# Performance work log

Measured on AMD Instinct MI355X. Metric: run time of the kernel, lower is better.

The kernel has to match this reference:

```python
import jax, jax.numpy as jnp
import numpy as np
from functools import partial

PI = 3.141592653589793

def prelu(x, a):
    return jnp.where(x > 0, x, a.reshape(()) * x)

def conv(x, w, b, stride=1):
    # torch Conv2d(k=3, padding=1): explicit (1,1) padding
    y = jax.lax.conv_general_dilated(
        x, w, window_strides=(stride, stride), padding=((1, 1), (1, 1)),
        dimension_numbers=("NCHW", "OIHW", "NCHW"))
    return y + b[None, :, None, None]

def feature_extractor(x, p):
    x = prelu(conv(x, p["w1"], p["b1"], 1), p["a1"])
    x1 = prelu(conv(x, p["w2"], p["b2"], 1), p["a2"])
    x = prelu(conv(x1, p["w3"], p["b3"], 2), p["a3"])
    x2 = prelu(conv(x, p["w4"], p["b4"], 1), p["a4"])
    x = prelu(conv(x2, p["w5"], p["b5"], 2), p["a5"])
    x3 = prelu(conv(x, p["w6"], p["b6"], 1), p["a6"])
    return x1, x2, x3

def cal_inter_flow(flo, sigma, t):
    # quadratic flow interpolation: circular-arc model with chord d, half-angle beta
    fx, fy = flo[:, 0:1], flo[:, 1:2]
    alpha = jnp.arctan2(fy, fx)
    beta = jnp.arcsin(sigma)
    d = jnp.sqrt(fx * fx + fy * fy)
    mask = jnp.abs(sigma) < 0.01            # near-linear motion branch
    safe_sig = jnp.where(mask, 1.0, sigma)
    R = jnp.where(mask, 0.0, d / (2.0 * safe_sig))
    th0 = alpha + PI / 2 + beta
    th1 = alpha + PI / 2 - beta
    tht = th0 + (th1 - th0) * t
    ftx = jnp.where(mask, t * fx, R * (jnp.cos(tht) - jnp.cos(th0)))
    fty = jnp.where(mask, t * fy, R * (jnp.sin(tht) - jnp.sin(th0)))
    return jnp.concatenate([ftx, fty], axis=1)

def flow_scale(flo, shape):
    # F.interpolate(bilinear, align_corners=False) then rescale flow magnitudes
    B = flo.shape[0]
    h, w = shape
    f = jax.image.resize(flo, (B, 2, h, w), method="bilinear")
    scale = jnp.asarray([w / flo.shape[3], h / flo.shape[2]], f.dtype).reshape(1, 2, 1, 1)
    return f * scale

def forward_warp(feat, flow):
    # 'average' forward splatting: bilinear scatter-add of values and weights, then normalize
    B, C, H, W = feat.shape
    gy, gx = jnp.meshgrid(jnp.arange(H, dtype=feat.dtype), jnp.arange(W, dtype=feat.dtype), indexing="ij")
    tx = gx[None] + flow[:, 0]              # [B,H,W] target coords
    ty = gy[None] + flow[:, 1]
    x0 = jnp.floor(tx); y0 = jnp.floor(ty)
    dx = tx - x0; dy = ty - y0
    x0i = x0.astype(jnp.int32); y0i = y0.astype(jnp.int32)
    featf = feat.reshape(B, C, H * W)
    num = jnp.zeros((B, C, H * W), feat.dtype)
    den = jnp.zeros((B, 1, H * W), feat.dtype)
    bidx = jnp.arange(B)[:, None, None]
    cidx = jnp.arange(C)[None, :, None]
    c0 = jnp.zeros((1, 1, 1), jnp.int32)
    corners = [
        (x0i,     y0i,     (1 - dx) * (1 - dy)),
        (x0i + 1, y0i,     dx * (1 - dy)),
        (x0i,     y0i + 1, (1 - dx) * dy),
        (x0i + 1, y0i + 1, dx * dy),
    ]
    for xi, yi, wgt in corners:
        valid = (xi >= 0) & (xi < W) & (yi >= 0) & (yi < H)
        wgt = (wgt * valid).reshape(B, 1, H * W)
        idx = (jnp.clip(yi, 0, H - 1) * W + jnp.clip(xi, 0, W - 1)).reshape(B, 1, H * W)
        num = num.at[bidx, cidx, idx].add(featf * wgt)
        den = den.at[bidx, c0, idx].add(wgt)
    out = num / jnp.maximum(den, 1e-7)
    return out.reshape(B, C, H, W)

def _forward(img0, img1, flow01, sigma01, flow10, sigma10, p):
    t = 0.5
    mean = jnp.concatenate([img0, img1], 1).mean(axis=(1, 2, 3), keepdims=True)
    img0 = img0 - mean
    img1 = img1 - mean
    flow_0t = cal_inter_flow(flow01, sigma01, t)
    flow_1t = cal_inter_flow(flow10, sigma10, 1 - t)
    f01, f02, f03 = feature_extractor(img0, p)
    f11, f12, f13 = feature_extractor(img1, p)
    fl0_d = flow_scale(flow_0t, f01.shape[2:]); fl1_d = flow_scale(flow_1t, f11.shape[2:])
    fl0_dd = flow_scale(flow_0t, f02.shape[2:]); fl1_dd = flow_scale(flow_1t, f12.shape[2:])
    fl0_ddd = flow_scale(flow_0t, f03.shape[2:]); fl1_ddd = flow_scale(flow_1t, f13.shape[2:])
    img_0t = forward_warp(img0, fl0_d);  img_1t = forward_warp(img1, fl1_d)
    ft0_1 = forward_warp(f01, fl0_d);    ft1_1 = forward_warp(f11, fl1_d)
    ft0_2 = forward_warp(f02, fl0_dd);   ft1_2 = forward_warp(f12, fl1_dd)
    ft0_3 = forward_warp(f03, fl0_ddd);  ft1_3 = forward_warp(f13, fl1_ddd)
    sig_0t = forward_warp(sigma01, flow_0t); sig_1t = forward_warp(sigma10, flow_1t)
    outs = [
        jnp.concatenate([img_0t, img_1t], 1),
        jnp.concatenate([ft0_1, ft1_1], 1),
        jnp.concatenate([ft0_2, ft1_2], 1),
        jnp.concatenate([ft0_3, ft1_3], 1),
        jnp.concatenate([sig_0t, sig_1t], 1),
    ]
    return jnp.concatenate([o.reshape(-1) for o in outs])

def setup_inputs() -> dict:
    key = jax.random.key(0)
    ks = jax.random.split(key, 16)
    B, H, W = 4, 256, 448
    inp = {
        "img0": jax.random.normal(ks[0], (B, 3, H, W), jnp.float32),
        "img1": jax.random.normal(ks[1], (B, 3, H, W), jnp.float32),
        "flow01": jax.random.normal(ks[2], (B, 2, H, W), jnp.float32) * 3.0,
        "sigma01": jax.random.uniform(ks[3], (B, 1, H, W), jnp.float32, -0.9, 0.9),
        "flow10": jax.random.normal(ks[4], (B, 2, H, W), jnp.float32) * 3.0,
        "sigma10": jax.random.uniform(ks[5], (B, 1, H, W), jnp.float32, -0.9, 0.9),
    }
    chans = [(32, 3), (32, 32), (64, 32), (64, 64), (96, 64), (96, 96)]
    for i, (o, c) in enumerate(chans, 1):
        inp[f"w{i}"] = jax.random.normal(ks[5 + i], (o, c, 3, 3), jnp.float32) * 0.05
        inp[f"b{i}"] = jnp.zeros((o,), jnp.float32)
        inp[f"a{i}"] = 0.25 * jnp.ones((1,), jnp.float32)
    return inp

def reference(img0, img1, flow01, sigma01, flow10, sigma10,
              w1, b1, a1, w2, b2, a2, w3, b3, a3,
              w4, b4, a4, w5, b5, a5, w6, b6, a6):
    p = dict(w1=w1, b1=b1, a1=a1, w2=w2, b2=b2, a2=a2, w3=w3, b3=b3, a3=a3,
             w4=w4, b4=b4, a4=a4, w5=w5, b5=b5, a5=a5, w6=w6, b6=b6, a6=a6)
    return _forward(img0, img1, flow01, sigma01, flow10, sigma10, p)
```

## Files before the change

### kernel.cpp

```cpp
#include <hip/hip_runtime.h>
#include <hip/hip_fp16.h>

static constexpr int B  = 4;
static constexpr int H0 = 256, W0 = 448, HW0 = H0 * W0;
static constexpr int H1 = 128, W1 = 224, HW1 = H1 * W1;
static constexpr int H2 = 64,  W2 = 112, HW2 = H2 * W2;

typedef _Float16 half8_t __attribute__((ext_vector_type(8)));
typedef _Float16 half4_t __attribute__((ext_vector_type(4)));
typedef float floatx4 __attribute__((ext_vector_type(4)));

static constexpr int NC_F = (W0 + 1) * (H0 + 1);
static constexpr int NC_H = (W1 + 1) * (H1 + 1);
static constexpr int NC_Q = (W2 + 1) * (H2 + 1);

static constexpr int RS_F = 20;
static constexpr int RS_H = 36;
static constexpr int RS_Q = 52;

static constexpr int SZ_F = 2 * B * NC_F;
static constexpr int SZ_H = 2 * B * NC_H;
static constexpr int SZ_Q = 2 * B * NC_Q;
static constexpr int CNT_TOTAL = SZ_F + SZ_H + SZ_Q;

static constexpr int CHUNK = 16384;
static constexpr int NCH_F = (SZ_F + CHUNK - 1) / CHUNK;
static constexpr int NCH_H = (SZ_H + CHUNK - 1) / CHUNK;
static constexpr int NCH_Q = (SZ_Q + CHUNK - 1) / CHUNK;
static constexpr int NCHUNKS = NCH_F + NCH_H + NCH_Q;

static constexpr size_t OFF_MEAN   = 0;
static constexpr size_t OFF_CNT    = 256;
static constexpr size_t ZERO_FLOATS = OFF_CNT + CNT_TOTAL;
static constexpr size_t OFF_BUFA   = ZERO_FLOATS;
static constexpr size_t OFF_BUFB   = OFF_BUFA + (size_t)4 * 32 * HW0;
static constexpr size_t OFF_FLOW   = OFF_BUFB + (size_t)4 * 32 * HW0;
static constexpr size_t OFF_FLH    = OFF_FLOW + (size_t)2 * B * 2 * HW0;
static constexpr size_t OFF_FLQ    = OFF_FLH + (size_t)2 * B * 2 * HW1;
static constexpr size_t OFF_WT2 = OFF_FLQ + (size_t)2 * B * 2 * HW2;
static constexpr size_t OFF_WT3 = OFF_WT2 + 4608;
static constexpr size_t OFF_WT4 = OFF_WT3 + 9216;
static constexpr size_t OFF_WT5 = OFF_WT4 + 18432;
static constexpr size_t OFF_WT6 = OFF_WT5 + 27648;
static constexpr size_t OFF_CS   = OFF_WT6 + 41472;
static constexpr size_t OFF_CURS = OFF_CS + (size_t)2 * CNT_TOTAL;
static constexpr size_t OFF_TPRE = OFF_CURS + CNT_TOTAL;
static constexpr size_t OFF_PSUM = OFF_TPRE + (size_t)NCHUNKS * 256;
static constexpr size_t OFF_RECS = OFF_PSUM + 128;
static constexpr size_t WS_FLOATS = OFF_RECS + (size_t)2 * B * HW0 * RS_F;

static constexpr size_t O_IMG = 0;
static constexpr size_t O_F1  = O_IMG + (size_t)B * 6 * HW0;
static constexpr size_t O_F2  = O_F1  + (size_t)B * 64 * HW0;
static constexpr size_t O_F3  = O_F2  + (size_t)B * 128 * HW1;
static constexpr size_t O_SIG = O_F3  + (size_t)B * 192 * HW2;

__device__ inline void h2f(unsigned u, float& lo, float& hi) {
  __half2 h = *reinterpret_cast<__half2*>(&u);
  float2 f = __half22float2(h);
  lo = f.x; hi = f.y;
}
__device__ inline unsigned f2h(float lo, float hi) {
  __half2 h = __floats2half2_rn(lo, hi);
  return *reinterpret_cast<unsigned*>(&h);
}

__device__ inline void chunk_map(int b, int& off, int& sz, int& ci) {
  if (b < NCH_F)              { off = 0;           sz = SZ_F; ci = b; }
  else if (b < NCH_F + NCH_H) { off = SZ_F;        sz = SZ_H; ci = b - NCH_F; }
  else                        { off = SZ_F + SZ_H; sz = SZ_Q; ci = b - NCH_F - NCH_H; }
}

__global__ __launch_bounds__(256) void k_mean(const float* __restrict__ img0,
                                              const float* __restrict__ img1,
                                              float* __restrict__ msum, int perImg) {
  int b = blockIdx.y;
  float s = 0.f;
  int tot = 2 * perImg;
  for (int i = blockIdx.x * blockDim.x + threadIdx.x; i < tot; i += gridDim.x * blockDim.x) {
    s += (i < perImg) ? img0[(size_t)b * perImg + i] : img1[(size_t)b * perImg + (i - perImg)];
  }
#pragma unroll
  for (int o = 32; o > 0; o >>= 1) s += __shfl_down(s, o);
  __shared__ float red[4];
  int lane = threadIdx.x & 63, wid = threadIdx.x >> 6;
  if (lane == 0) red[wid] = s;
  __syncthreads();
  if (threadIdx.x == 0) atomicAdd(&msum[b], red[0] + red[1] + red[2] + red[3]);
}

__global__ __launch_bounds__(256) void k_interflow2(
    const float* __restrict__ f01, const float* __restrict__ s01,
    const float* __restrict__ f10, const float* __restrict__ s10,
    float* __restrict__ outBase, unsigned* __restrict__ cntF) {
  constexpr int NCX = W0 + 1;
  int i = blockIdx.x * 256 + threadIdx.x;
  if (i >= 2 * B * HW0) return;
  int nb = i / HW0;
  int px = i - nb * HW0;
  int dir = nb >> 2, b = nb & 3;
  const float* flo = dir ? f10 : f01;
  const float* sigma = dir ? s10 : s01;
  float fx = flo[((size_t)(b * 2 + 0)) * HW0 + px];
  float fy = flo[((size_t)(b * 2 + 1)) * HW0 + px];
  float sg = sigma[(size_t)b * HW0 + px];
  float ftx, fty;
  if (fabsf(sg) < 0.01f) {
    ftx = 0.5f * fx; fty = 0.5f * fy;
  } else {
    float g = (1.f - sqrtf(fmaxf(0.f, 1.f - sg * sg))) / (2.f * sg);
    ftx = 0.5f * fx - g * fy;
    fty = 0.5f * fy + g * fx;
  }
  outBase[((size_t)(nb * 2 + 0)) * HW0 + px] = ftx;
  outBase[((size_t)(nb * 2 + 1)) * HW0 + px] = fty;
  int sw = px % W0, sh = px / W0;
  float tx = (float)sw + ftx, ty = (float)sh + fty;
  int x0 = (int)floorf(tx), y0 = (int)floorf(ty);
  if (x0 >= -1 && x0 <= W0 - 1 && y0 >= -1 && y0 <= H0 - 1)
    atomicAdd(&cntF[nb * NC_F + (y0 + 1) * NCX + (x0 + 1)], 1u);
}

template <int F, int Hd, int Wd>
__global__ __launch_bounds__(256) void k_downflow2(
    const float* __restrict__ in, float* __restrict__ out,
    unsigned* __restrict__ cnt) {
  constexpr int HWd = Hd * Wd;
  constexpr int NCX = Wd + 1;
  constexpr int NC  = (Wd + 1) * (Hd + 1);
  int i = blockIdx.x * 256 + threadIdx.x;
  if (i >= 2 * B * HWd) return;
  int nb = i / HWd;
  int px = i - nb * HWd;
  int ow = px % Wd, oh = px / Wd;
  float cy = (oh + 0.5f) * F - 0.5f;
  float cx = (ow + 0.5f) * F - 0.5f;
  int ylo = (int)floorf(cy) - F + 1;
  int xlo = (int)floorf(cx) - F + 1;
  const float* ipx = in + ((size_t)(nb * 2 + 0)) * HW0;
  const float* ipy = in + ((size_t)(nb * 2 + 1)) * HW0;
  float ax = 0.f, ay = 0.f, wn = 0.f;
  for (int jy = 0; jy < 2 * F; jy++) {
    int y = ylo + jy;
    if ((unsigned)y >= (unsigned)H0) continue;
    float wy = 1.f - fabsf((float)y - cy) / (float)F;
    for (int jx = 0; jx < 2 * F; jx++) {
      int x = xlo + jx;
      if ((unsigned)x >= (unsigned)W0) continue;
      float wx = 1.f - fabsf((float)x - cx) / (float)F;
      float ww = wy * wx;
      ax += ww * ipx[(size_t)y * W0 + x];
      ay += ww * ipy[(size_t)y * W0 + x];
      wn += ww;
    }
  }
  float s = 1.f / (wn * (float)F);
  float fx = ax * s, fy = ay * s;
  out[((size_t)(nb * 2 + 0)) * HWd + px] = fx;
  out[((size_t)(nb * 2 + 1)) * HWd + px] = fy;
  float tx = (float)ow + fx, ty = (float)oh + fy;
  int x0 = (int)floorf(tx), y0 = (int)floorf(ty);
  if (x0 >= -1 && x0 <= Wd - 1 && y0 >= -1 && y0 <= Hd - 1)
    atomicAdd(&cnt[nb * NC + (y0 + 1) * NCX + (x0 + 1)], 1u);
}

__global__ __launch_bounds__(256) void k_wtrans_all(
    const float* __restrict__ w2, const float* __restrict__ w3,
    const float* __restrict__ w4, const float* __restrict__ w5,
    const float* __restrict__ w6,
    _Float16* __restrict__ o2, _Float16* __restrict__ o3,
    _Float16* __restrict__ o4, _Float16* __restrict__ o5,
    _Float16* __restrict__ o6) {
  int i = blockIdx.x * 256 + threadIdx.x;
  const float* w; _Float16* o; int COUT, CIN, base;
  if      (i <   9216) { w = w2; o = o2; COUT = 32; CIN = 32; base = 0; }
  else if (i <  27648) { w = w3; o = o3; COUT = 64; CIN = 32; base = 9216; }
  else if (i <  64512) { w = w4; o = o4; COUT = 64; CIN = 64; base = 27648; }
  else if (i < 119808) { w = w5; o = o5; COUT = 96; CIN = 64; base = 64512; }
  else if (i < 202752) { w = w6; o = o6; COUT = 96; CIN = 96; base = 119808; }
  else return;
  int j = i - base;
  int q = j % 9;
  int rest = j / 9;
  int ci = rest % CIN;
  int co = rest / CIN;
  o[((size_t)q * COUT + co) * CIN + ci] = (_Float16)w[j];
}

__global__ __launch_bounds__(256) void conv1_nhwc(
    const float* __restrict__ img0, const float* __restrict__ img1,
    const float* __restrict__ msum, float invCnt,
    const float* __restrict__ wgt, const float* __restrict__ bias,
    const float* __restrict__ alpha, _Float16* __restrict__ outp) {
  __shared__ float wsm[32 * 27];
  __shared__ float bsm[32];
  int n = blockIdx.z;
  for (int i = threadIdx.x; i < 32 * 27; i += 256) wsm[i] = wgt[i];
  if (threadIdx.x < 32) bsm[threadIdx.x] = bias[threadIdx.x];
  __syncthreads();
  int b = n & 3;
  const float* ip = (n < 4 ? img0 : img1) + (size_t)b * 3 * HW0;
  float m = msum[b] * invCnt;
  int tx = blockIdx.x % 7, ty = blockIdx.x / 7;
  int ow = tx * 64 + (threadIdx.x & 63);
  int oh = ty * 4 + (threadIdx.x >> 6);
  float xv[27];
#pragma unroll
  for (int ci = 0; ci < 3; ci++) {
    const float* iq = ip + (size_t)ci * HW0;
#pragma unroll
    for (int ky = 0; ky < 3; ky++) {
      int y = oh - 1 + ky;
      bool yv = (unsigned)y < (unsigned)H0;
      const float* row = iq + (size_t)y * W0;
#pragma unroll
      for (int kx = 0; kx < 3; kx++) {
        int x = ow - 1 + kx;
        xv[ci * 9 + ky * 3 + kx] = (yv && (unsigned)x < (unsigned)W0) ? row[x] - m : 0.f;
      }
    }
  }
  float a = alpha[0];
  _Float16* ob = outp + ((size_t)(n * H0 + oh) * W0 + ow) * 32;
#pragma clang loop unroll(disable)
  for (int g = 0; g < 4; g++) {
    float acc[8];
#pragma unroll
    for (int k = 0; k < 8; k++) acc[k] = bsm[g * 8 + k];
#pragma unroll
    for (int k = 0; k < 8; k++) {
      const float* wp = &wsm[(g * 8 + k) * 27];
#pragma unroll
      for (int j = 0; j < 27; j++) acc[k] += xv[j] * wp[j];
    }
    half8_t h;
#pragma unroll
    for (int k = 0; k < 8; k++) {
      float v = acc[k];
      v = v > 0.f ? v : a * v;
      h[k] = (_Float16)v;
    }
    *(half8_t*)(ob + g * 8) = h;
  }
}

template <int CIN, int COUT, int STRIDE, int TROWS>
__global__ __launch_bounds__(256) void conv_mfma(
    const _Float16* __restrict__ in, const _Float16* __restrict__ wT,
    const float* __restrict__ bias, const float* __restrict__ alpha,
    _Float16* __restrict__ outp, int Hin, int Win, int Hout, int Wout) {
  int gx = gridDim.x, gy = gridDim.y, gz = gridDim.z;
  int T = gx * gy * gz;
  int lb = ((int)blockIdx.z * gy + blockIdx.y) * gx + blockIdx.x;
  lb = (lb & 7) * (T >> 3) + (lb >> 3);
  int cob  = lb % gy;
  int n    = (lb / gy) % gz;
  int tile = lb / (gy * gz);
  int lane = threadIdx.x & 63, wave = threadIdx.x >> 6;
  int l15 = lane & 15, lhi = lane >> 4;
  int tiles_x = Wout >> 4;
  int tx = tile % tiles_x, ty = tile / tiles_x;
  int ow0 = tx << 4;
  int oh0 = ty * (4 * TROWS) + wave * TROWS;
  int co0 = cob * 32;
  floatx4 acc[2][TROWS] = {};
  const _Float16* ip = in + (size_t)n * Hin * Win * CIN;
  int x_base = (ow0 + l15) * STRIDE;
  int ybase = oh0 * STRIDE - 1;
  constexpr int NY = (TROWS - 1) * STRIDE + 3;
  const _Float16* wA = wT + (size_t)(co0 + l15) * CIN;
  const _Float16* wB = wT + (size_t)(co0 + 16 + l15) * CIN;
  for (int kc = 0; kc < CIN / 32; kc++) {
    int ci = kc * 32 + lhi * 8;
#pragma unroll
    for (int dxi = 0; dxi < 3; dxi++) {
      int x = x_base + dxi - 1;
      bool xv = (unsigned)x < (unsigned)Win;
      int xc = x < 0 ? 0 : (x >= Win ? Win - 1 : x);
      half8_t a0[3], a1[3];
#pragma unroll
      for (int dy = 0; dy < 3; dy++) {
        int q = dy * 3 + dxi;
        a0[dy] = *(const half8_t*)(wA + (size_t)q * COUT * CIN + ci);
        a1[dy] = *(const half8_t*)(wB + (size_t)q * COUT * CIN + ci);
      }
#pragma unroll
      for (int y6 = 0; y6 < NY; y6++) {
        int y = ybase + y6;
        if ((unsigned)y >= (unsigned)Hin) continue;
        half8_t bf = *(const half8_t*)(ip + ((size_t)y * Win + xc) * CIN + ci);
        half8_t z = {};
        bf = xv ? bf : z;
#pragma unroll
        for (int dy = 0; dy < 3; dy++) {
          int tnum = y6 - dy;
          if (tnum < 0 || tnum % STRIDE != 0) continue;
          int t = tnum / STRIDE;
          if (t >= TROWS) continue;
          acc[0][t] = __builtin_amdgcn_mfma_f32_16x16x32_f16(a0[dy], bf, acc[0][t], 0, 0, 0);
          acc[1][t] = __builtin_amdgcn_mfma_f32_16x16x32_f16(a1[dy], bf, acc[1][t], 0, 0, 0);
        }
      }
    }
  }
  float aP = alpha[0];
#pragma unroll
  for (int h = 0; h < 2; h++) {
    float bia[4];
#pragma unroll
    for (int r = 0; r < 4; r++) bia[r] = bias[co0 + h * 16 + lhi * 4 + r];
#pragma unroll
    for (int t = 0; t < TROWS; t++) {
      half4_t hh;
#pragma unroll
      for (int r = 0; r < 4; r++) {
        float v = acc[h][t][r] + bia[r];
        v = v > 0.f ? v : aP * v;
        hh[r] = (_Float16)v;
      }
      *(half4_t*)(outp + (((size_t)n * Hout + oh0 + t) * Wout + ow0 + l15) * COUT +
                  co0 + h * 16 + lhi * 4) = hh;
    }
  }
}

__global__ __launch_bounds__(256) void k_scan_part(
    const unsigned* __restrict__ cnt, unsigned* __restrict__ tpre,
    unsigned* __restrict__ psum) {
  int b = blockIdx.x, t = threadIdx.x;
  int off, sz, ci;
  chunk_map(b, off, sz, ci);
  int base = off + ci * CHUNK + t * 64;
  int lim = off + min(sz, (ci + 1) * CHUNK);
  unsigned s = 0;
  for (int j = 0; j < 64; j++) {
    int idx = base + j;
    if (idx < lim) s += cnt[idx];
  }
  __shared__ unsigned sm[256];
  sm[t] = s;
  __syncthreads();
  for (int o = 1; o < 256; o <<= 1) {
    unsigned v = (t >= o) ? sm[t - o] : 0u;
    __syncthreads();
    sm[t] += v;
    __syncthreads();
  }
  unsigned incl = sm[t];
  tpre[b * 256 + t] = incl - s;
  if (t == 255) psum[b] = incl;
}

__global__ __launch_bounds__(256) void k_scan_apply(
    const unsigned* __restrict__ cnt, const unsigned* __restrict__ tpre,
    const unsigned* __restrict__ psum,
    uint2* __restrict__ cs, unsigned* __restrict__ curs) {
  int b = blockIdx.x, t = threadIdx.x;
  int off, sz, ci;
  chunk_map(b, off, sz, ci);
  __shared__ unsigned cbs;
  if (t == 0) {
    int first = (off == 0) ? 0 : (off == SZ_F ? NCH_F : NCH_F + NCH_H);
    unsigned c = 0;
    for (int k = first; k < first + ci; k++) c += psum[k];
    cbs = c;
  }
  __syncthreads();
  int base = off + ci * CHUNK + t * 64;
  int lim = off + min(sz, (ci + 1) * CHUNK);
  unsigned run = cbs + tpre[b * 256 + t];
  for (int j = 0; j < 64; j++) {
    int idx = base + j;
    if (idx < lim) {
      unsigned c = cnt[idx];
      cs[idx] = make_uint2(run, c);
      curs[idx] = run;
      run += c;
    }
  }
}

__global__ __launch_bounds__(256) void k_pack_full(
    const float* __restrict__ img0, const float* __restrict__ img1,
    const float* __restrict__ msum, float invCnt,
    const _Float16* __restrict__ featN,
    const float* __restrict__ s01, const float* __restrict__ s10,
    const float* __restrict__ flowB,
    float* __restrict__ recs, unsigned* __restrict__ curs) {
  constexpr int NCX = W0 + 1;
  int px = blockIdx.x * 256 + threadIdx.x;
  int b = blockIdx.y;
  int dir = blockIdx.z;
  if (px >= HW0) return;
  int nb = dir * B + b;
  float fx = flowB[((size_t)(nb * 2 + 0)) * HW0 + px];
  float fy = flowB[((size_t)(nb * 2 + 1)) * HW0 + px];
  int sw = px % W0, sh = px / W0;
  float tx = (float)sw + fx, ty = (float)sh + fy;
  float x0f = floorf(tx), y0f = floorf(ty);
  int x0 = (int)x0f, y0 = (int)y0f;
  if (x0 < -1 || x0 > W0 - 1 || y0 < -1 || y0 > H0 - 1) return;
  const float* imp = (dir ? img1 : img0) + (size_t)b * 3 * HW0;
  float m = msum[b] * invCnt;
  float im0 = imp[px] - m, im1 = imp[(size_t)HW0 + px] - m, im2 = imp[(size_t)2 * HW0 + px] - m;
  const float* sig = dir ? s10 : s01;
  float sg = sig[(size_t)b * HW0 + px];
  union { floatx4 f4[RS_F / 4]; unsigned u[RS_F]; } r;
  r.u[0] = f2h(im0, im1);
  r.u[1] = f2h(im2, sg);
  const floatx4* fp = (const floatx4*)(featN + ((size_t)nb * HW0 + px) * 32);
  union { floatx4 f; unsigned u[4]; } t;
#pragma unroll
  for (int j = 0; j < 4; j++) {
    t.f = fp[j];
    r.u[2 + 4 * j + 0] = t.u[0]; r.u[2 + 4 * j + 1] = t.u[1];
    r.u[2 + 4 * j + 2] = t.u[2]; r.u[2 + 4 * j + 3] = t.u[3];
  }
  r.u[18] = __float_as_uint(tx - x0f);
  r.u[19] = __float_as_uint(ty - y0f);
  unsigned slot = atomicAdd(&curs[nb * NC_F + (y0 + 1) * NCX + (x0 + 1)], 1u);
  floatx4* o = (floatx4*)(recs + (size_t)slot * RS_F);
#pragma unroll
  for (int j = 0; j < RS_F / 4; j++) o[j] = r.f4[j];
}

template <int C, int Hd, int Wd, int RS>
__global__ __launch_bounds__(256) void k_pack_feat(
    const _Float16* __restrict__ featN, const float* __restrict__ flowB,
    float* __restrict__ recs, unsigned* __restrict__ curs) {
  constexpr int HWd = Hd * Wd;
  constexpr int NCX = Wd + 1;
  constexpr int NC  = (Wd + 1) * (Hd + 1);
  int px = blockIdx.x * 256 + threadIdx.x;
  int b = blockIdx.y;
  int dir = blockIdx.z;
  if (px >= HWd) return;
  int nb = dir * B + b;
  float fx = flowB[((size_t)(nb * 2 + 0)) * HWd + px];
  float fy = flowB[((size_t)(nb * 2 + 1)) * HWd + px];
  int sw = px % Wd, sh = px / Wd;
  float tx = (float)sw + fx, ty = (float)sh + fy;
  float x0f = floorf(tx), y0f = floorf(ty);
  int x0 = (int)x0f, y0 = (int)y0f;
  if (x0 < -1 || x0 > Wd - 1 || y0 < -1 || y0 > Hd - 1) return;
  union { floatx4 f4[RS / 4]; unsigned u[RS]; } r;
  const floatx4* fp = (const floatx4*)(featN + ((size_t)nb * HWd + px) * C);
#pragma unroll
  for (int j = 0; j < C / 8; j++) r.f4[j] = fp[j];
  r.u[C / 2]     = __float_as_uint(tx - x0f);
  r.u[C / 2 + 1] = __float_as_uint(ty - y0f);
#pragma unroll
  for (int j = C / 2 + 2; j < RS; j++) r.u[j] = 0;
  unsigned slot = atomicAdd(&curs[nb * NC + (y0 + 1) * NCX + (x0 + 1)], 1u);
  floatx4* o = (floatx4*)(recs + (size_t)slot * RS);
#pragma unroll
  for (int j = 0; j < RS / 4; j++) o[j] = r.f4[j];
}

__global__ __launch_bounds__(256) void k_warp_gather_full(
    const float* __restrict__ recs, const uint2* __restrict__ cs,
    float* __restrict__ outImg, float* __restrict__ outFeat, float* __restrict__ outSig) {
  constexpr int NCX = W0 + 1;
  int gx = gridDim.x;
  int T = gx * gridDim.y * gridDim.z;
  int lb = ((int)blockIdx.z * gridDim.y + blockIdx.y) * gx + blockIdx.x;
  lb = (lb & 7) * (T >> 3) + (lb >> 3);
  int q = (lb % gx) * 256 + (int)threadIdx.x;
  int b = (lb / gx) % B;
  int dir = lb / (gx * B);
  if (q >= HW0) return;
  int nb = dir * B + b;
  int qx = q % W0, qy = q / W0;
  float acc[36];
#pragma unroll
  for (int c = 0; c < 36; c++) acc[c] = 0.f;
  float dsum = 0.f;
  for (int ky = 0; ky < 2; ky++) {
    int cy = qy - 1 + ky;
    for (int kx = 0; kx < 2; kx++) {
      int cx = qx - 1 + kx;
      uint2 sc = cs[nb * NC_F + (cy + 1) * NCX + (cx + 1)];
      unsigned s0 = sc.x, cn = sc.y;
      for (unsigned s = s0; s < s0 + cn; s++) {
        const floatx4* r4 = (const floatx4*)(recs + (size_t)s * RS_F);
        floatx4 a0 = r4[0], a1 = r4[1], a2 = r4[2], a3 = r4[3], a4 = r4[4];
        union { floatx4 f; unsigned u[4]; } t;
        float ch[36]; float dxf, dyf;
        t.f = a0; h2f(t.u[0], ch[0], ch[1]);   h2f(t.u[1], ch[2], ch[35]);
                  h2f(t.u[2], ch[3], ch[4]);   h2f(t.u[3], ch[5], ch[6]);
        t.f = a1; h2f(t.u[0], ch[7], ch[8]);   h2f(t.u[1], ch[9], ch[10]);
                  h2f(t.u[2], ch[11], ch[12]); h2f(t.u[3], ch[13], ch[14]);
        t.f = a2; h2f(t.u[0], ch[15], ch[16]); h2f(t.u[1], ch[17], ch[18]);
                  h2f(t.u[2], ch[19], ch[20]); h2f(t.u[3], ch[21], ch[22]);
        t.f = a3; h2f(t.u[0], ch[23], ch[24]); h2f(t.u[1], ch[25], ch[26]);
                  h2f(t.u[2], ch[27], ch[28]); h2f(t.u[3], ch[29], ch[30]);
        t.f = a4; h2f(t.u[0], ch[31], ch[32]); h2f(t.u[1], ch[33], ch[34]);
        dxf = __uint_as_float(t.u[2]); dyf = __uint_as_float(t.u[3]);
        float wx = kx ? (1.f - dxf) : dxf;
        float wy = ky ? (1.f - dyf) : dyf;
        float w = wx * wy;
        dsum += w;
#pragma unroll
        for (int c = 0; c < 36; c++) acc[c] += w * ch[c];
      }
    }
  }
  float inv = 1.f / fmaxf(dsum, 1e-7f);
#pragma unroll
  for (int c = 0; c < 3; c++)
    outImg[((size_t)(b * 6 + dir * 3 + c)) * HW0 + q] = acc[c] * inv;
#pragma unroll
  for (int c = 0; c < 32; c++)
    outFeat[((size_t)(b * 64 + dir * 32 + c)) * HW0 + q] = acc[3 + c] * inv;
  outSig[((size_t)(b * 2 + dir)) * HW0 + q] = acc[35] * inv;
}

template <int C, int Hd, int Wd, int RS, int Z>
__global__ __launch_bounds__(256) void k_warp_gather_feat(
    const float* __restrict__ recs, const uint2* __restrict__ cs,
    float* __restrict__ outF) {
  constexpr int HWd = Hd * Wd;
  constexpr int NCX = Wd + 1;
  constexpr int NC  = (Wd + 1) * (Hd + 1);
  int gx = gridDim.x;
  int T = gx * gridDim.y * gridDim.z;
  int lb = ((int)blockIdx.z * gridDim.y + blockIdx.y) * gx + blockIdx.x;
  lb = (lb & 7) * (T >> 3) + (lb >> 3);
  int q = (lb % gx) * 256 + (int)threadIdx.x;
  int b = (lb / gx) % B;
  int dz = lb / (gx * B);
  int z = dz % Z, dir = dz / Z;
  int c0 = z * 32;
  if (q >= HWd) return;
  int nb = dir * B + b;
  int qx = q % Wd, qy = q / Wd;
  float acc[32];
#pragma unroll
  for (int c = 0; c < 32; c++) acc[c] = 0.f;
  float dsum = 0.f;
  for (int ky = 0; ky < 2; ky++) {
    int cy = qy - 1 + ky;
    for (int kx = 0; kx < 2; kx++) {
      int cx = qx - 1 + kx;
      uint2 sc = cs[nb * NC + (cy + 1) * NCX + (cx + 1)];
      unsigned s0 = sc.x, cn = sc.y;
      for (unsigned s = s0; s < s0 + cn; s++) {
        const unsigned* rp = (const unsigned*)(recs + (size_t)s * RS);
        const floatx4* r4 = (const floatx4*)rp;
        floatx4 a0 = r4[4 * z + 0], a1 = r4[4 * z + 1], a2 = r4[4 * z + 2], a3 = r4[4 * z + 3];
        float2 hd = *(const float2*)(rp + C / 2);
        union { floatx4 f; unsigned u[4]; } t;
        float ch[32];
        t.f = a0; h2f(t.u[0], ch[0], ch[1]);  h2f(t.u[1], ch[2], ch[3]);
                  h2f(t.u[2], ch[4], ch[5]);  h2f(t.u[3], ch[6], ch[7]);
        t.f = a1; h2f(t.u[0], ch[8], ch[9]);  h2f(t.u[1], ch[10], ch[11]);
                  h2f(t.u[2], ch[12], ch[13]);h2f(t.u[3], ch[14], ch[15]);
        t.f = a2; h2f(t.u[0], ch[16], ch[17]);h2f(t.u[1], ch[18], ch[19]);
                  h2f(t.u[2], ch[20], ch[21]);h2f(t.u[3], ch[22], ch[23]);
        t.f = a3; h2f(t.u[0], ch[24], ch[25]);h2f(t.u[1], ch[26], ch[27]);
                  h2f(t.u[2], ch[28], ch[29]);h2f(t.u[3], ch[30], ch[31]);
        float dxf = hd.x, dyf = hd.y;
        float wx = kx ? (1.f - dxf) : dxf;
        float wy = ky ? (1.f - dyf) : dyf;
        float w = wx * wy;
        dsum += w;
#pragma unroll
        for (int c = 0; c < 32; c++) acc[c] += w * ch[c];
      }
    }
  }
  float inv = 1.f / fmaxf(dsum, 1e-7f);
  size_t obase = ((size_t)(b * 2 * C + dir * C + c0)) * HWd + q;
#pragma unroll
  for (int c = 0; c < 32; c++) outF[obase + (size_t)c * HWd] = acc[c] * inv;
}

extern "C" void kernel_launch(void* const* d_in, const int* in_sizes, int n_in,
                              void* d_out, int out_size, void* d_ws, size_t ws_size,
                              hipStream_t stream) {
  (void)in_sizes; (void)n_in; (void)out_size;
  if (ws_size < WS_FLOATS * sizeof(float)) return;

  const float* img0    = (const float*)d_in[0];
  const float* img1    = (const float*)d_in[1];
  const float* flow01  = (const float*)d_in[2];
  const float* sigma01 = (const float*)d_in[3];
  const float* flow10  = (const float*)d_in[4];
  const float* sigma10 = (const float*)d_in[5];
  const float* wp[6]; const float* bp[6]; const float* ap[6];
  for (int i = 0; i < 6; i++) {
    wp[i] = (const float*)(d_in[6 + 3 * i]);
    bp[i] = (const float*)(d_in[7 + 3 * i]);
    ap[i] = (const float*)(d_in[8 + 3 * i]);
  }
  float* ws  = (float*)d_ws;
  float* out = (float*)d_out;

  unsigned* cntAll  = (unsigned*)(ws + OFF_CNT);
  unsigned* cntF = cntAll;
  unsigned* cntH = cntAll + SZ_F;
  unsigned* cntQ = cntAll + SZ_F + SZ_H;
  uint2*    csAll = (uint2*)(ws + OFF_CS);
  uint2*    csF = csAll, *csH = csAll + SZ_F, *csQ = csAll + SZ_F + SZ_H;
  unsigned* cursAll  = (unsigned*)(ws + OFF_CURS);
  unsigned* cursF = cursAll, *cursH = cursAll + SZ_F, *cursQ = cursAll + SZ_F + SZ_H;
  unsigned* tpre  = (unsigned*)(ws + OFF_TPRE);
  unsigned* psum  = (unsigned*)(ws + OFF_PSUM);
  float*    recs    = ws + OFF_RECS;
  _Float16* Ah = (_Float16*)(ws + OFF_BUFA);
  _Float16* Bh = (_Float16*)(ws + OFF_BUFB);
  _Float16* wt[5] = {(_Float16*)(ws + OFF_WT2), (_Float16*)(ws + OFF_WT3),
                     (_Float16*)(ws + OFF_WT4), (_Float16*)(ws + OFF_WT5),
                     (_Float16*)(ws + OFF_WT6)};
  float* flowF = ws + OFF_FLOW;
  float* flowH = ws + OFF_FLH;
  float* flowQ = ws + OFF_FLQ;

  const float invCnt = 1.f / (6.f * (float)HW0);

  hipMemsetAsync(ws, 0, ZERO_FLOATS * sizeof(float), stream);

  dim3 blk(256);

  k_wtrans_all<<<dim3((202752 + 255) / 256), blk, 0, stream>>>(
      wp[1], wp[2], wp[3], wp[4], wp[5], wt[0], wt[1], wt[2], wt[3], wt[4]);

  k_mean<<<dim3(32, B), blk, 0, stream>>>(img0, img1, ws + OFF_MEAN, 3 * HW0);

  k_interflow2<<<dim3((2 * B * HW0 + 255) / 256), blk, 0, stream>>>(
      flow01, sigma01, flow10, sigma10, flowF, cntF);
  k_downflow2<2, H1, W1><<<dim3((2 * B * HW1 + 255) / 256), blk, 0, stream>>>(
      flowF, flowH, cntH);
  k_downflow2<4, H2, W2><<<dim3((2 * B * HW2 + 255) / 256), blk, 0, stream>>>(
      flowF, flowQ, cntQ);

  k_scan_part<<<dim3(NCHUNKS), blk, 0, stream>>>(cntAll, tpre, psum);
  k_scan_apply<<<dim3(NCHUNKS), blk, 0, stream>>>(cntAll, tpre, psum, csAll, cursAll);

  conv1_nhwc<<<dim3(7 * 64, 1, 8), blk, 0, stream>>>(
      img0, img1, ws + OFF_MEAN, invCnt, wp[0], bp[0], ap[0], Ah);
  conv_mfma<32, 32, 1, 8><<<dim3(28 * 8, 1, 8), blk, 0, stream>>>(
      Ah, wt[0], bp[1], ap[1], Bh, H0, W0, H0, W0);

  k_pack_full<<<dim3(HW0 / 256, B, 2), blk, 0, stream>>>(
      img0, img1, ws + OFF_MEAN, invCnt, Bh, sigma01, sigma10, flowF, recs, cursF);
  k_warp_gather_full<<<dim3(HW0 / 256, B, 2), blk, 0, stream>>>(
      recs, csF, out + O_IMG, out + O_F1, out + O_SIG);

  conv_mfma<32, 64, 2, 4><<<dim3(14 * 8, 2, 8), blk, 0, stream>>>(
      Bh, wt[1], bp[2], ap[2], Ah, H0, W0, H1, W1);
  conv_mfma<64, 64, 1, 8><<<dim3(14 * 4, 2, 8), blk, 0, stream>>>(
      Ah, wt[2], bp[3], ap[3], Bh, H1, W1, H1, W1);

  k_pack_feat<64, H1, W1, RS_H><<<dim3(HW1 / 256, B, 2), blk, 0, stream>>>(
      Bh, flowH, recs, cursH);
  k_warp_gather_feat<64, H1, W1, RS_H, 2><<<dim3(HW1 / 256, B, 4), blk, 0, stream>>>(
      recs, csH, out + O_F2);

  conv_mfma<64, 96, 2, 4><<<dim3(7 * 4, 3, 8), blk, 0, stream>>>(
      Bh, wt[3], bp[4], ap[4], Ah, H1, W1, H2, W2);
  conv_mfma<96, 96, 1, 4><<<dim3(7 * 4, 3, 8), blk, 0, stream>>>(
      Ah, wt[4], bp[5], ap[5], Bh, H2, W2, H2, W2);

  k_pack_feat<96, H2, W2, RS_Q><<<dim3(HW2 / 256, B, 2), blk, 0, stream>>>(
      Bh, flowQ, recs, cursQ);
  k_warp_gather_feat<96, H2, W2, RS_Q, 3><<<dim3(HW2 / 256, B, 6), blk, 0, stream>>>(
      recs, csQ, out + O_F3);
}
```

Before: 643.8 us.

## Fuse independent stages into combined launches to overlap warp and conv work

Turns the separate stage kernels into device functions. Independent stages share one launch and are dispatched by block index: interflow+mean+weight transpose, downflow+conv1, scan_part+conv2, pack+conv3, gather+conv4, and so on. This cuts the launch count and lets the memory-bound splat/gather work run alongside the MFMA convolutions instead of serializing. In exchange, each fused kernel takes the worst-case register and LDS footprint of its branches, which may lower occupancy for the lighter stage.

```diff
diff --git a/kernel.cpp b/kernel.cpp
--- a/kernel.cpp
+++ b/kernel.cpp
@@ -55,6 +55,22 @@
 static constexpr size_t O_F3  = O_F2  + (size_t)B * 128 * HW1;
 static constexpr size_t O_SIG = O_F3  + (size_t)B * 192 * HW2;
 
+static constexpr int NB_IF = 2 * B * HW0 / 256;
+static constexpr int NB_MEAN = 32 * B;
+static constexpr int NB_WT = (202752 + 255) / 256;
+static constexpr int NB_DH = 2 * B * HW1 / 256;
+static constexpr int NB_DQ = 2 * B * HW2 / 256;
+static constexpr int NB_C1 = 448 * 8;
+static constexpr int NB_C2 = 224 * 8;
+static constexpr int NB_PF = (HW0 / 256) * B * 2;
+static constexpr int NB_C3 = 112 * 2 * 8;
+static constexpr int NB_GF = NB_PF;
+static constexpr int NB_C4 = 56 * 2 * 8;
+static constexpr int NB_PH = (HW1 / 256) * B * 2;
+static constexpr int NB_C5 = 28 * 3 * 8;
+static constexpr int NB_GH = (HW1 / 256) * B * 4;
+static constexpr int NB_C6 = 28 * 3 * 8;
+
 __device__ inline void h2f(unsigned u, float& lo, float& hi) {
   __half2 h = *reinterpret_cast<__half2*>(&u);
   float2 f = __half22float2(h);
@@ -71,30 +87,32 @@
   else                        { off = SZ_F + SZ_H; sz = SZ_Q; ci = b - NCH_F - NCH_H; }
 }
 
-__global__ __launch_bounds__(256) void k_mean(const float* __restrict__ img0,
-                                              const float* __restrict__ img1,
-                                              float* __restrict__ msum, int perImg) {
-  int b = blockIdx.y;
-  float s = 0.f;
+
+__device__ __forceinline__ void d_mean(const float* __restrict__ img0,
+                                       const float* __restrict__ img1,
+                                       float* __restrict__ msum, int s) {
+  const int perImg = 3 * HW0;
+  int bx = s & 31, b = s >> 5;
+  float acc = 0.f;
   int tot = 2 * perImg;
-  for (int i = blockIdx.x * blockDim.x + threadIdx.x; i < tot; i += gridDim.x * blockDim.x) {
-    s += (i < perImg) ? img0[(size_t)b * perImg + i] : img1[(size_t)b * perImg + (i - perImg)];
-  }
-#pragma unroll
-  for (int o = 32; o > 0; o >>= 1) s += __shfl_down(s, o);
+  for (int i = bx * 256 + threadIdx.x; i < tot; i += 32 * 256) {
+    acc += (i < perImg) ? img0[(size_t)b * perImg + i] : img1[(size_t)b * perImg + (i - perImg)];
+  }
+#pragma unroll
+  for (int o = 32; o > 0; o >>= 1) acc += __shfl_down(acc, o);
   __shared__ float red[4];
   int lane = threadIdx.x & 63, wid = threadIdx.x >> 6;
-  if (lane == 0) red[wid] = s;
+  if (lane == 0) red[wid] = acc;
   __syncthreads();
   if (threadIdx.x == 0) atomicAdd(&msum[b], red[0] + red[1] + red[2] + red[3]);
 }
 
-__global__ __launch_bounds__(256) void k_interflow2(
+__device__ __forceinline__ void d_interflow2(
     const float* __restrict__ f01, const float* __restrict__ s01,
     const float* __restrict__ f10, const float* __restrict__ s10,
-    float* __restrict__ outBase, unsigned* __restrict__ cntF) {
+    float* __restrict__ outBase, unsigned* __restrict__ cntF, int s) {
   constexpr int NCX = W0 + 1;
-  int i = blockIdx.x * 256 + threadIdx.x;
+  int i = s * 256 + (int)threadIdx.x;
   if (i >= 2 * B * HW0) return;
   int nb = i / HW0;
   int px = i - nb * HW0;
@@ -122,13 +140,13 @@
 }
 
 template <int F, int Hd, int Wd>
-__global__ __launch_bounds__(256) void k_downflow2(
+__device__ __forceinline__ void d_downflow2(
     const float* __restrict__ in, float* __restrict__ out,
-    unsigned* __restrict__ cnt) {
+    unsigned* __restrict__ cnt, int s) {
   constexpr int HWd = Hd * Wd;
   constexpr int NCX = Wd + 1;
   constexpr int NC  = (Wd + 1) * (Hd + 1);
-  int i = blockIdx.x * 256 + threadIdx.x;
+  int i = s * 256 + (int)threadIdx.x;
   if (i >= 2 * B * HWd) return;
   int nb = i / HWd;
   int px = i - nb * HWd;
@@ -154,8 +172,8 @@
       wn += ww;
     }
   }
-  float s = 1.f / (wn * (float)F);
-  float fx = ax * s, fy = ay * s;
+  float sc = 1.f / (wn * (float)F);
+  float fx = ax * sc, fy = ay * sc;
   out[((size_t)(nb * 2 + 0)) * HWd + px] = fx;
   out[((size_t)(nb * 2 + 1)) * HWd + px] = fy;
   float tx = (float)ow + fx, ty = (float)oh + fy;
@@ -164,14 +182,14 @@
     atomicAdd(&cnt[nb * NC + (y0 + 1) * NCX + (x0 + 1)], 1u);
 }
 
-__global__ __launch_bounds__(256) void k_wtrans_all(
+__device__ __forceinline__ void d_wtrans(
     const float* __restrict__ w2, const float* __restrict__ w3,
     const float* __restrict__ w4, const float* __restrict__ w5,
     const float* __restrict__ w6,
     _Float16* __restrict__ o2, _Float16* __restrict__ o3,
     _Float16* __restrict__ o4, _Float16* __restrict__ o5,
-    _Float16* __restrict__ o6) {
-  int i = blockIdx.x * 256 + threadIdx.x;
+    _Float16* __restrict__ o6, int s) {
+  int i = s * 256 + (int)threadIdx.x;
   const float* w; _Float16* o; int COUT, CIN, base;
   if      (i <   9216) { w = w2; o = o2; COUT = 32; CIN = 32; base = 0; }
   else if (i <  27648) { w = w3; o = o3; COUT = 64; CIN = 32; base = 9216; }
@@ -187,21 +205,21 @@
   o[((size_t)q * COUT + co) * CIN + ci] = (_Float16)w[j];
 }
 
-__global__ __launch_bounds__(256) void conv1_nhwc(
+__device__ __forceinline__ void d_conv1(
     const float* __restrict__ img0, const float* __restrict__ img1,
     const float* __restrict__ msum, float invCnt,
     const float* __restrict__ wgt, const float* __restrict__ bias,
-    const float* __restrict__ alpha, _Float16* __restrict__ outp) {
+    const float* __restrict__ alpha, _Float16* __restrict__ outp, int s) {
   __shared__ float wsm[32 * 27];
   __shared__ float bsm[32];
-  int n = blockIdx.z;
+  int bx = s % 448, n = s / 448;
   for (int i = threadIdx.x; i < 32 * 27; i += 256) wsm[i] = wgt[i];
   if (threadIdx.x < 32) bsm[threadIdx.x] = bias[threadIdx.x];
   __syncthreads();
   int b = n & 3;
   const float* ip = (n < 4 ? img0 : img1) + (size_t)b * 3 * HW0;
   float m = msum[b] * invCnt;
-  int tx = blockIdx.x % 7, ty = blockIdx.x / 7;
+  int tx = bx % 7, ty = bx / 7;
   int ow = tx * 64 + (threadIdx.x & 63);
   int oh = ty * 4 + (threadIdx.x >> 6);
   float xv[27];
@@ -245,13 +263,12 @@
 }
 
 template <int CIN, int COUT, int STRIDE, int TROWS>
-__global__ __launch_bounds__(256) void conv_mfma(
+__device__ __forceinline__ void conv_mfma_body(
     const _Float16* __restrict__ in, const _Float16* __restrict__ wT,
     const float* __restrict__ bias, const float* __restrict__ alpha,
-    _Float16* __restrict__ outp, int Hin, int Win, int Hout, int Wout) {
-  int gx = gridDim.x, gy = gridDim.y, gz = gridDim.z;
+    _Float16* __restrict__ outp, int Hin, int Win, int Hout, int Wout,
+    int gx, int gy, int gz, int lb) {
   int T = gx * gy * gz;
-  int lb = ((int)blockIdx.z * gy + blockIdx.y) * gx + blockIdx.x;
   lb = (lb & 7) * (T >> 3) + (lb >> 3);
   int cob  = lb % gy;
   int n    = (lb / gy) % gz;
@@ -324,10 +341,10 @@
   }
 }
 
-__global__ __launch_bounds__(256) void k_scan_part(
+__device__ __forceinline__ void d_scan_part(
     const unsigned* __restrict__ cnt, unsigned* __restrict__ tpre,
-    unsigned* __restrict__ psum) {
-  int b = blockIdx.x, t = threadIdx.x;
+    unsigned* __restrict__ psum, int b) {
+  int t = threadIdx.x;
   int off, sz, ci;
   chunk_map(b, off, sz, ci);
   int base = off + ci * CHUNK + t * 64;
@@ -351,47 +368,18 @@
   if (t == 255) psum[b] = incl;
 }
 
-__global__ __launch_bounds__(256) void k_scan_apply(
-    const unsigned* __restrict__ cnt, const unsigned* __restrict__ tpre,
-    const unsigned* __restrict__ psum,
-    uint2* __restrict__ cs, unsigned* __restrict__ curs) {
-  int b = blockIdx.x, t = threadIdx.x;
-  int off, sz, ci;
-  chunk_map(b, off, sz, ci);
-  __shared__ unsigned cbs;
-  if (t == 0) {
-    int first = (off == 0) ? 0 : (off == SZ_F ? NCH_F : NCH_F + NCH_H);
-    unsigned c = 0;
-    for (int k = first; k < first + ci; k++) c += psum[k];
-    cbs = c;
-  }
-  __syncthreads();
-  int base = off + ci * CHUNK + t * 64;
-  int lim = off + min(sz, (ci + 1) * CHUNK);
-  unsigned run = cbs + tpre[b * 256 + t];
-  for (int j = 0; j < 64; j++) {
-    int idx = base + j;
-    if (idx < lim) {
-      unsigned c = cnt[idx];
-      cs[idx] = make_uint2(run, c);
-      curs[idx] = run;
-      run += c;
-    }
-  }
-}
-
-__global__ __launch_bounds__(256) void k_pack_full(
+__device__ __forceinline__ void pack_full_body(
     const float* __restrict__ img0, const float* __restrict__ img1,
     const float* __restrict__ msum, float invCnt,
     const _Float16* __restrict__ featN,
     const float* __restrict__ s01, const float* __restrict__ s10,
     const float* __restrict__ flowB,
-    float* __restrict__ recs, unsigned* __restrict__ curs) {
+    float* __restrict__ recs, unsigned* __restrict__ curs, int s) {
   constexpr int NCX = W0 + 1;
-  int px = blockIdx.x * 256 + threadIdx.x;
-  int b = blockIdx.y;
-  int dir = blockIdx.z;
-  if (px >= HW0) return;
+  constexpr int GX = HW0 / 256;
+  int px = (s % GX) * 256 + (int)threadIdx.x;
+  int b = (s / GX) % B;
+  int dir = s / (GX * B);
   int nb = dir * B + b;
   float fx = flowB[((size_t)(nb * 2 + 0)) * HW0 + px];
   float fy = flowB[((size_t)(nb * 2 + 1)) * HW0 + px];
@@ -425,16 +413,16 @@
 }
 
 template <int C, int Hd, int Wd, int RS>
-__global__ __launch_bounds__(256) void k_pack_feat(
+__device__ __forceinline__ void pack_feat_body(
     const _Float16* __restrict__ featN, const float* __restrict__ flowB,
-    float* __restrict__ recs, unsigned* __restrict__ curs) {
+    float* __restrict__ recs, unsigned* __restrict__ curs, int s) {
   constexpr int HWd = Hd * Wd;
   constexpr int NCX = Wd + 1;
   constexpr int NC  = (Wd + 1) * (Hd + 1);
-  int px = blockIdx.x * 256 + threadIdx.x;
-  int b = blockIdx.y;
-  int dir = blockIdx.z;
-  if (px >= HWd) return;
+  constexpr int GX = HWd / 256;
+  int px = (s % GX) * 256 + (int)threadIdx.x;
+  int b = (s / GX) % B;
+  int dir = s / (GX * B);
   int nb = dir * B + b;
   float fx = flowB[((size_t)(nb * 2 + 0)) * HWd + px];
   float fy = flowB[((size_t)(nb * 2 + 1)) * HWd + px];
@@ -457,18 +445,17 @@
   for (int j = 0; j < RS / 4; j++) o[j] = r.f4[j];
 }
 
-__global__ __launch_bounds__(256) void k_warp_gather_full(
+__device__ __forceinline__ void gather_full_body(
     const float* __restrict__ recs, const uint2* __restrict__ cs,
-    float* __restrict__ outImg, float* __restrict__ outFeat, float* __restrict__ outSig) {
+    float* __restrict__ outImg, float* __restrict__ outFeat,
+    float* __restrict__ outSig, int lb) {
   constexpr int NCX = W0 + 1;
-  int gx = gridDim.x;
-  int T = gx * gridDim.y * gridDim.z;
-  int lb = ((int)blockIdx.z * gridDim.y + blockIdx.y) * gx + blockIdx.x;
+  constexpr int GX = HW0 / 256;
+  constexpr int T = GX * B * 2;
   lb = (lb & 7) * (T >> 3) + (lb >> 3);
-  int q = (lb % gx) * 256 + (int)threadIdx.x;
-  int b = (lb / gx) % B;
-  int dir = lb / (gx * B);
-  if (q >= HW0) return;
+  int q = (lb % GX) * 256 + (int)threadIdx.x;
+  int b = (lb / GX) % B;
+  int dir = lb / (GX * B);
   int nb = dir * B + b;
   int qx = q % W0, qy = q / W0;
   float acc[36];
@@ -516,22 +503,20 @@
 }
 
 template <int C, int Hd, int Wd, int RS, int Z>
-__global__ __launch_bounds__(256) void k_warp_gather_feat(
+__device__ __forceinline__ void gather_feat_body(
     const float* __restrict__ recs, const uint2* __restrict__ cs,
-    float* __restrict__ outF) {
+    float* __restrict__ outF, int lb) {
   constexpr int HWd = Hd * Wd;
   constexpr int NCX = Wd + 1;
   constexpr int NC  = (Wd + 1) * (Hd + 1);
-  int gx = gridDim.x;
-  int T = gx * gridDim.y * gridDim.z;
-  int lb = ((int)blockIdx.z * gridDim.y + blockIdx.y) * gx + blockIdx.x;
+  constexpr int GX = HWd / 256;
+  constexpr int T = GX * B * 2 * Z;
   lb = (lb & 7) * (T >> 3) + (lb >> 3);
-  int q = (lb % gx) * 256 + (int)threadIdx.x;
-  int b = (lb / gx) % B;
-  int dz = lb / (gx * B);
+  int q = (lb % GX) * 256 + (int)threadIdx.x;
+  int b = (lb / GX) % B;
+  int dz = lb / (GX * B);
   int z = dz % Z, dir = dz / Z;
   int c0 = z * 32;
-  if (q >= HWd) return;
   int nb = dir * B + b;
   int qx = q % Wd, qy = q / Wd;
   float acc[32];
@@ -575,6 +560,127 @@
   for (int c = 0; c < 32; c++) outF[obase + (size_t)c * HWd] = acc[c] * inv;
 }
 
+
+__global__ __launch_bounds__(256) void k_front(
+    const float* f01, const float* s01, const float* f10, const float* s10,
+    float* flowF, unsigned* cntF,
+    const float* img0, const float* img1, float* msum,
+    const float* w2, const float* w3, const float* w4, const float* w5, const float* w6,
+    _Float16* o2, _Float16* o3, _Float16* o4, _Float16* o5, _Float16* o6) {
+  int f = blockIdx.x;
+  if (f < NB_IF) d_interflow2(f01, s01, f10, s10, flowF, cntF, f);
+  else if (f < NB_IF + NB_MEAN) d_mean(img0, img1, msum, f - NB_IF);
+  else d_wtrans(w2, w3, w4, w5, w6, o2, o3, o4, o5, o6, f - NB_IF - NB_MEAN);
+}
+
+__global__ __launch_bounds__(256) void k_down_conv1(
+    const float* flowF, float* flowH, unsigned* cntH, float* flowQ, unsigned* cntQ,
+    const float* img0, const float* img1, const float* msum, float invCnt,
+    const float* w1, const float* b1, const float* a1, _Float16* Ah) {
+  int f = blockIdx.x;
+  if (f < NB_DH) d_downflow2<2, H1, W1>(flowF, flowH, cntH, f);
+  else if (f < NB_DH + NB_DQ) d_downflow2<4, H2, W2>(flowF, flowQ, cntQ, f - NB_DH);
+  else d_conv1(img0, img1, msum, invCnt, w1, b1, a1, Ah, f - NB_DH - NB_DQ);
+}
+
+__global__ __launch_bounds__(256) void k_scan_conv2(
+    const unsigned* cntAll, unsigned* tpre, unsigned* psum,
+    const _Float16* Ah, const _Float16* wt2, const float* b2, const float* a2,
+    _Float16* Bh) {
+  int f = blockIdx.x;
+  if (f < NCHUNKS) d_scan_part(cntAll, tpre, psum, f);
+  else conv_mfma_body<32, 32, 1, 8>(Ah, wt2, b2, a2, Bh, H0, W0, H0, W0,
+                                    224, 1, 8, f - NCHUNKS);
+}
+
+__global__ __launch_bounds__(256) void k_scan_apply(
+    const unsigned* __restrict__ cnt, const unsigned* __restrict__ tpre,
+    const unsigned* __restrict__ psum,
+    uint2* __restrict__ cs, unsigned* __restrict__ curs) {
+  int b = blockIdx.x, t = threadIdx.x;
+  int off, sz, ci;
+  chunk_map(b, off, sz, ci);
+  __shared__ unsigned cbs;
+  if (t == 0) {
+    int first = (off == 0) ? 0 : (off == SZ_F ? NCH_F : NCH_F + NCH_H);
+    unsigned c = 0;
+    for (int k = first; k < first + ci; k++) c += psum[k];
+    cbs = c;
+  }
+  __syncthreads();
+  int base = off + ci * CHUNK + t * 64;
+  int lim = off + min(sz, (ci + 1) * CHUNK);
+  unsigned run = cbs + tpre[b * 256 + t];
+  for (int j = 0; j < 64; j++) {
+    int idx = base + j;
+    if (idx < lim) {
+      unsigned c = cnt[idx];
+      cs[idx] = make_uint2(run, c);
+      curs[idx] = run;
+      run += c;
+    }
+  }
+}
+
+__global__ __launch_bounds__(256) void k_packF_conv3(
+    const float* img0, const float* img1, const float* msum, float invCnt,
+    const _Float16* Bh, const float* s01, const float* s10, const float* flowF,
+    float* recs, unsigned* cursF,
+    const _Float16* wt3, const float* b3, const float* a3, _Float16* Ah) {
+  int f = blockIdx.x;
+  if (f < NB_PF)
+    pack_full_body(img0, img1, msum, invCnt, Bh, s01, s10, flowF, recs, cursF, f);
+  else
+    conv_mfma_body<32, 64, 2, 4>(Bh, wt3, b3, a3, Ah, H0, W0, H1, W1,
+                                 112, 2, 8, f - NB_PF);
+}
+
+__global__ __launch_bounds__(256) void k_gatherF_conv4(
+    const float* recs, const uint2* csF,
+    float* outImg, float* outFeat, float* outSig,
+    const _Float16* Ah, const _Float16* wt4, const float* b4, const float* a4,
+    _Float16* Bh) {
+  int f = blockIdx.x;
+  if (f < NB_GF)
+    gather_full_body(recs, csF, outImg, outFeat, outSig, f);
+  else
+    conv_mfma_body<64, 64, 1, 8>(Ah, wt4, b4, a4, Bh, H1, W1, H1, W1,
+                                 56, 2, 8, f - NB_GF);
+}
+
+__global__ __launch_bounds__(256) void k_packH_conv5(
+    const _Float16* Bh, const float* flowH, float* recs, unsigned* cursH,
+    const _Float16* wt5, const float* b5, const float* a5, _Float16* Ah) {
+  int f = blockIdx.x;
+  if (f < NB_PH)
+    pack_feat_body<64, H1, W1, RS_H>(Bh, flowH, recs, cursH, f);
+  else
+    conv_mfma_body<64, 96, 2, 4>(Bh, wt5, b5, a5, Ah, H1, W1, H2, W2,
+                                 28, 3, 8, f - NB_PH);
+}
+
+__global__ __launch_bounds__(256) void k_gatherH_conv6(
+    const float* recs, const uint2* csH, float* outF2,
+    const _Float16* Ah, const _Float16* wt6, const float* b6, const float* a6,
+    _Float16* Bh) {
+  int f = blockIdx.x;
+  if (f < NB_GH)
+    gather_feat_body<64, H1, W1, RS_H, 2>(recs, csH, outF2, f);
+  else
+    conv_mfma_body<96, 96, 1, 4>(Ah, wt6, b6, a6, Bh, H2, W2, H2, W2,
+                                 28, 3, 8, f - NB_GH);
+}
+
+__global__ __launch_bounds__(256) void k_packQ(
+    const _Float16* Bh, const float* flowQ, float* recs, unsigned* cursQ) {
+  pack_feat_body<96, H2, W2, RS_Q>(Bh, flowQ, recs, cursQ, blockIdx.x);
+}
+
+__global__ __launch_bounds__(256) void k_gatherQ(
+    const float* recs, const uint2* csQ, float* outF3) {
+  gather_feat_body<96, H2, W2, RS_Q, 3>(recs, csQ, outF3, blockIdx.x);
+}
+
 extern "C" void kernel_launch(void* const* d_in, const int* in_sizes, int n_in,
                               void* d_out, int out_size, void* d_ws, size_t ws_size,
                               hipStream_t stream) {
@@ -606,7 +712,7 @@
   unsigned* cursF = cursAll, *cursH = cursAll + SZ_F, *cursQ = cursAll + SZ_F + SZ_H;
   unsigned* tpre  = (unsigned*)(ws + OFF_TPRE);
   unsigned* psum  = (unsigned*)(ws + OFF_PSUM);
-  float*    recs    = ws + OFF_RECS;
+  float*    recs  = ws + OFF_RECS;
   _Float16* Ah = (_Float16*)(ws + OFF_BUFA);
   _Float16* Bh = (_Float16*)(ws + OFF_BUFB);
   _Float16* wt[5] = {(_Float16*)(ws + OFF_WT2), (_Float16*)(ws + OFF_WT3),
@@ -622,48 +728,34 @@
 
   dim3 blk(256);
 
-  k_wtrans_all<<<dim3((202752 + 255) / 256), blk, 0, stream>>>(
+  k_front<<<dim3(NB_IF + NB_MEAN + NB_WT), blk, 0, stream>>>(
+      flow01, sigma01, flow10, sigma10, flowF, cntF,
+      img0, img1, ws + OFF_MEAN,
       wp[1], wp[2], wp[3], wp[4], wp[5], wt[0], wt[1], wt[2], wt[3], wt[4]);
 
-  k_mean<<<dim3(32, B), blk, 0, stream>>>(img0, img1, ws + OFF_MEAN, 3 * HW0);
-
-  k_interflow2<<<dim3((2 * B * HW0 + 255) / 256), blk, 0, stream>>>(
-      flow01, sigma01, flow10, sigma10, flowF, cntF);
-  k_downflow2<2, H1, W1><<<dim3((2 * B * HW1 + 255) / 256), blk, 0, stream>>>(
-      flowF, flowH, cntH);
-  k_downflow2<4, H2, W2><<<dim3((2 * B * HW2 + 255) / 256), blk, 0, stream>>>(
-      flowF, flowQ, cntQ);
-
-  k_scan_part<<<dim3(NCHUNKS), blk, 0, stream>>>(cntAll, tpre, psum);
+  k_down_conv1<<<dim3(NB_DH + NB_DQ + NB_C1), blk, 0, stream>>>(
+      flowF, flowH, cntH, flowQ, cntQ,
+      img0, img1, ws + OFF_MEAN, invCnt, wp[0], bp[0], ap[0], Ah);
+
+  k_scan_conv2<<<dim3(NCHUNKS + NB_C2), blk, 0, stream>>>(
+      cntAll, tpre, psum, Ah, wt[0], bp[1], ap[1], Bh);
+
   k_scan_apply<<<dim3(NCHUNKS), blk, 0, stream>>>(cntAll, tpre, psum, csAll, cursAll);
 
-  conv1_nhwc<<<dim3(7 * 64, 1, 8), blk, 0, stream>>>(
-      img0, img1, ws + OFF_MEAN, invCnt, wp[0], bp[0], ap[0], Ah);
-  conv_mfma<32, 32, 1, 8><<<dim3(28 * 8, 1, 8), blk, 0, stream>>>(
-      Ah, wt[0], bp[1], ap[1], Bh, H0, W0, H0, W0);
-
-  k_pack_full<<<dim3(HW0 / 256, B, 2), blk, 0, stream>>>(
-      img0, img1, ws + OFF_MEAN, invCnt, Bh, sigma01, sigma10, flowF, recs, cursF);
-  k_warp_gather_full<<<dim3(HW0 / 256, B, 2), blk, 0, stream>>>(
-      recs, csF, out + O_IMG, out + O_F1, out + O_SIG);
-
-  conv_mfma<32, 64, 2, 4><<<dim3(14 * 8, 2, 8), blk, 0, stream>>>(
-      Bh, wt[1], bp[2], ap[2], Ah, H0, W0, H1, W1);
-  conv_mfma<64, 64, 1, 8><<<dim3(14 * 4, 2, 8), blk, 0, stream>>>(
-      Ah, wt[2], bp[3], ap[3], Bh, H1, W1, H1, W1);
-
-  k_pack_feat<64, H1, W1, RS_H><<<dim3(HW1 / 256, B, 2), blk, 0, stream>>>(
-      Bh, flowH, recs, cursH);
-  k_warp_gather_feat<64, H1, W1, RS_H, 2><<<dim3(HW1 / 256, B, 4), blk, 0, stream>>>(
-      recs, csH, out + O_F2);
-
-  conv_mfma<64, 96, 2, 4><<<dim3(7 * 4, 3, 8), blk, 0, stream>>>(
-      Bh, wt[3], bp[4], ap[4], Ah, H1, W1, H2, W2);
-  conv_mfma<96, 96, 1, 4><<<dim3(7 * 4, 3, 8), blk, 0, stream>>>(
-      Ah, wt[4], bp[5], ap[5], Bh, H2, W2, H2, W2);
-
-  k_pack_feat<96, H2, W2, RS_Q><<<dim3(HW2 / 256, B, 2), blk, 0, stream>>>(
-      Bh, flowQ, recs, cursQ);
-  k_warp_gather_feat<96, H2, W2, RS_Q, 3><<<dim3(HW2 / 256, B, 6), blk, 0, stream>>>(
-      recs, csQ, out + O_F3);
-}
+  k_packF_conv3<<<dim3(NB_PF + NB_C3), blk, 0, stream>>>(
+      img0, img1, ws + OFF_MEAN, invCnt, Bh, sigma01, sigma10, flowF,
+      recs, cursF, wt[1], bp[2], ap[2], Ah);
+
+  k_gatherF_conv4<<<dim3(NB_GF + NB_C4), blk, 0, stream>>>(
+      recs, csF, out + O_IMG, out + O_F1, out + O_SIG,
+      Ah, wt[2], bp[3], ap[3], Bh);
+
+  k_packH_conv5<<<dim3(NB_PH + NB_C5), blk, 0, stream>>>(
+      Bh, flowH, recs, cursH, wt[3], bp[4], ap[4], Ah);
+
+  k_gatherH_conv6<<<dim3(NB_GH + NB_C6), blk, 0, stream>>>(
+      recs, csH, out + O_F2, Ah, wt[4], bp[5], ap[5], Bh);
+
+  k_packQ<<<dim3((HW2 / 256) * B * 2), blk, 0, stream>>>(Bh, flowQ, recs, cursQ);
+  k_gatherQ<<<dim3((HW2 / 256) * B * 6), blk, 0, stream>>>(recs, csQ, out + O_F3);
+}
```

New measurement: 573.6 us. -10.9%, faster.
